# Kernel optimization log

Hardware: AMD Instinct MI355X
Metric: run time of the kernel (lower is better)

The kernel has to match this reference:

```python
import jax, jax.numpy as jnp
import numpy as np

B, S, D_IN = 1, 2048, 2048
H, KV, HD = 32, 8, 64          # num_heads, num_kv_groups, head_dim
GS = H // KV                    # group_size
D_OUT = H * HD
EPS = 1e-6


def _rmsnorm(x, w):
    # RMSNormQwen over last dim (head_dim)
    var = jnp.mean(x * x, axis=-1, keepdims=True)
    return x * jax.lax.rsqrt(var + EPS) * w


def _rope(x, cos, sin):
    # rotate-half RoPE; x: [B, heads, S, HD], cos/sin: [S, HD]
    d = x.shape[-1]
    x1, x2 = x[..., : d // 2], x[..., d // 2 :]
    rot = jnp.concatenate([-x2, x1], axis=-1)
    return x * cos + rot * sin


def setup_inputs() -> dict:
    key = jax.random.key(0)
    ks = jax.random.split(key, 8)
    x = jax.random.normal(ks[0], (B, S, D_IN), dtype=jnp.float32)
    Wq = jax.random.normal(ks[1], (D_IN, D_OUT), dtype=jnp.float32) * 0.02
    Wk = jax.random.normal(ks[2], (D_IN, KV * HD), dtype=jnp.float32) * 0.02
    Wv = jax.random.normal(ks[3], (D_IN, KV * HD), dtype=jnp.float32) * 0.02
    Wo = jax.random.normal(ks[4], (D_OUT, D_IN), dtype=jnp.float32) * 0.02
    q_norm_w = jnp.ones((HD,), dtype=jnp.float32)
    k_norm_w = jnp.ones((HD,), dtype=jnp.float32)
    # causal mask: True where masked (j > i)
    mask = jnp.triu(jnp.ones((S, S), dtype=bool), k=1)
    # RoPE tables
    inv_freq = 1.0 / (10000.0 ** (np.arange(0, HD, 2, dtype=np.float32) / HD))
    ang = np.arange(S, dtype=np.float32)[:, None] * inv_freq[None, :]  # [S, HD/2]
    cos = jnp.asarray(np.concatenate([np.cos(ang), np.cos(ang)], axis=-1))
    sin = jnp.asarray(np.concatenate([np.sin(ang), np.sin(ang)], axis=-1))
    return {"x": x, "mask": mask, "cos": cos, "sin": sin,
            "Wq": Wq, "Wk": Wk, "Wv": Wv, "Wo": Wo,
            "q_norm_w": q_norm_w, "k_norm_w": k_norm_w}


def reference(x, mask, cos, sin, Wq, Wk, Wv, Wo, q_norm_w, k_norm_w):
    b, s, _ = x.shape
    q = (x @ Wq).reshape(b, s, H, HD).transpose(0, 2, 1, 3)   # [B,H,S,HD]
    k = (x @ Wk).reshape(b, s, KV, HD).transpose(0, 2, 1, 3)  # [B,KV,S,HD]
    v = (x @ Wv).reshape(b, s, KV, HD).transpose(0, 2, 1, 3)  # [B,KV,S,HD]
    q = _rmsnorm(q, q_norm_w)
    k = _rmsnorm(k, k_norm_w)
    q = _rope(q, cos, sin)
    k = _rope(k, cos, sin)
    # grouped-KV attention without materializing repeated K/V
    qg = q.reshape(b, KV, GS, s, HD)
    scores = jnp.einsum('bkgsd,bktd->bkgst', qg, k)           # [B,KV,GS,S,S]
    scores = jnp.where(mask, -jnp.inf, scores)
    weights = jax.nn.softmax(scores / (HD ** 0.5), axis=-1)
    ctx = jnp.einsum('bkgst,bktd->bkgsd', weights, v)         # [B,KV,GS,S,HD]
    ctx = ctx.reshape(b, H, s, HD).transpose(0, 2, 1, 3).reshape(b, s, D_OUT)
    return ctx @ Wo
```

## Files before the change

### kernel.cpp

```cpp
#include <hip/hip_runtime.h>
#include <hip/hip_bf16.h>
#include <math.h>

#define S_LEN 2048
#define DIN   2048
#define NH    32
#define NKV   8
#define HD    64
#define DOUT  2048
#define QKVN  3072
#define KOFF  2048
#define VOFF  2560

typedef __attribute__((ext_vector_type(8))) short short8v;
typedef __attribute__((ext_vector_type(8))) unsigned short ushort8v;
typedef __attribute__((ext_vector_type(4))) unsigned short ushort4v;
typedef __attribute__((ext_vector_type(4))) float float4v;
typedef __attribute__((ext_vector_type(16))) float float16v;

__device__ __forceinline__ float bf2f(unsigned short u) {
    union { float f; unsigned u; } c; c.u = ((unsigned)u) << 16; return c.f;
}
__device__ __forceinline__ unsigned short f2bf(float f) {
    union { float f; unsigned u; } c; c.f = f;
    unsigned r = c.u + 0x7fffu + ((c.u >> 16) & 1u);
    return (unsigned short)(r >> 16);
}
__device__ __forceinline__ unsigned short f2h(float f) {
    union { _Float16 h; unsigned short u; } c; c.h = (_Float16)f; return c.u;
}
__device__ __forceinline__ float h2f(unsigned short u) {
    union { _Float16 h; unsigned short u; } c; c.u = u; return (float)c.h;
}
__device__ __forceinline__ unsigned cvtpk(float lo, float hi) {
    unsigned r;
    asm("v_cvt_pk_bf16_f32 %0, %1, %2" : "=v"(r) : "v"(lo), "v"(hi));
    return r;
}

__global__ __launch_bounds__(256) void prep(const float* __restrict__ Wq,
                                            const float* __restrict__ Wk,
                                            const float* __restrict__ Wv,
                                            const float* __restrict__ Wo,
                                            const float* __restrict__ x,
                                            unsigned short* __restrict__ W1,
                                            unsigned short* __restrict__ WoT,
                                            unsigned short* __restrict__ XB) {
    __shared__ float t[32][33];
    const int a = blockIdx.x;
    const int tx = threadIdx.x & 31, ty = threadIdx.x >> 5;
    if (a < 6144) {
        const int n0 = (a % 96) * 32, k0 = (a / 96) * 32;
        const float* src; int nn0, Nsrc;
        if (n0 < KOFF)      { src = Wq; nn0 = n0;        Nsrc = DOUT; }
        else if (n0 < VOFF) { src = Wk; nn0 = n0 - KOFF; Nsrc = 512; }
        else                { src = Wv; nn0 = n0 - VOFF; Nsrc = 512; }
#pragma unroll
        for (int j = ty; j < 32; j += 8)
            t[j][tx] = src[(size_t)(k0 + j) * Nsrc + nn0 + tx];
        __syncthreads();
#pragma unroll
        for (int j = ty; j < 32; j += 8)
            W1[(size_t)(n0 + j) * DIN + k0 + tx] = f2bf(t[tx][j]);
    } else if (a < 10240) {
        const int b = a - 6144;
        const int n0 = (b % 64) * 32, k0 = (b / 64) * 32;
#pragma unroll
        for (int j = ty; j < 32; j += 8)
            t[j][tx] = Wo[(size_t)(k0 + j) * DIN + n0 + tx];
        __syncthreads();
#pragma unroll
        for (int j = ty; j < 32; j += 8)
            WoT[(size_t)(n0 + j) * DOUT + k0 + tx] = f2bf(t[tx][j]);
    } else {
        const int i = (a - 10240) * 1024 + threadIdx.x * 4;
        float4 v = *(const float4*)(x + i);
        XB[i + 0] = f2bf(v.x); XB[i + 1] = f2bf(v.y);
        XB[i + 2] = f2bf(v.z); XB[i + 3] = f2bf(v.w);
    }
}

template <int FUSE>
__global__ __launch_bounds__(256) void gemm64(const unsigned short* __restrict__ A,
                                              const unsigned short* __restrict__ Bt,
                                              void* __restrict__ Cv, int M, int N, int K,
                                              const float* __restrict__ qnw,
                                              const float* __restrict__ knw,
                                              const float* __restrict__ cosb,
                                              const float* __restrict__ sinb) {
    __shared__ __attribute__((aligned(16))) unsigned short As[128 * 32];
    __shared__ __attribute__((aligned(16))) unsigned short Bs[64 * 32];
    const int tid = threadIdx.x, lane = tid & 63, w = tid >> 6;
    const int bm = blockIdx.y * 128, bn = blockIdx.x * 64;
    const int wm = w * 32;

    float4v acc[2][4];
#pragma unroll
    for (int i = 0; i < 2; i++)
#pragma unroll
        for (int j = 0; j < 4; j++) acc[i][j] = (float4v){0.f, 0.f, 0.f, 0.f};

    const int lr = lane >> 2, lc = (lane & 3) * 8;
    const unsigned short* Ag0 = A + (size_t)(bm + w * 32 + lr) * K + lc;
    const unsigned short* Ag1 = Ag0 + (size_t)16 * K;
    const unsigned short* Bg  = Bt + (size_t)(bn + w * 16 + lr) * K + lc;
    unsigned short* Al0 = As + (w * 32) * 32;
    unsigned short* Al1 = As + (w * 32 + 16) * 32;
    unsigned short* Bl  = Bs + (w * 16) * 32;

    const int frow = lane & 15, fk = (lane >> 4) * 8;

    for (int k0 = 0; k0 < K; k0 += 32) {
        __syncthreads();
        __builtin_amdgcn_global_load_lds(
            (const __attribute__((address_space(1))) void*)(Ag0 + k0),
            (__attribute__((address_space(3))) void*)Al0, 16, 0, 0);
        __builtin_amdgcn_global_load_lds(
            (const __attribute__((address_space(1))) void*)(Ag1 + k0),
            (__attribute__((address_space(3))) void*)Al1, 16, 0, 0);
        __builtin_amdgcn_global_load_lds(
            (const __attribute__((address_space(1))) void*)(Bg + k0),
            (__attribute__((address_space(3))) void*)Bl, 16, 0, 0);
        __syncthreads();

        short8v af[2], bf[4];
#pragma unroll
        for (int fm = 0; fm < 2; fm++)
            af[fm] = *(const short8v*)(As + (wm + fm * 16 + frow) * 32 + fk);
#pragma unroll
        for (int fn = 0; fn < 4; fn++)
            bf[fn] = *(const short8v*)(Bs + (fn * 16 + frow) * 32 + fk);
#pragma unroll
        for (int fm = 0; fm < 2; fm++)
#pragma unroll
            for (int fn = 0; fn < 4; fn++)
                acc[fm][fn] = __builtin_amdgcn_mfma_f32_16x16x32_bf16(
                    af[fm], bf[fn], acc[fm][fn], 0, 0, 0);
    }

    const int quad = lane >> 4, col16 = lane & 15;
    if constexpr (FUSE == 1) {
        unsigned short* C = (unsigned short*)Cv;
        const int head = bn >> 6;
        if (head < 40) {
            const float* nw = (head < 32) ? qnw : knw;
            float wv[4];
#pragma unroll
            for (int fn = 0; fn < 4; fn++) wv[fn] = nw[fn * 16 + col16];
#pragma unroll
            for (int fm = 0; fm < 2; fm++)
#pragma unroll
                for (int r = 0; r < 4; r++) {
                    float x0 = acc[fm][0][r], x1 = acc[fm][1][r];
                    float x2 = acc[fm][2][r], x3 = acc[fm][3][r];
                    float ss = x0 * x0 + x1 * x1 + x2 * x2 + x3 * x3;
                    ss += __shfl_xor(ss, 1); ss += __shfl_xor(ss, 2);
                    ss += __shfl_xor(ss, 4); ss += __shfl_xor(ss, 8);
                    const float inv = rsqrtf(ss * (1.0f / 64.0f) + 1e-6f);
                    float xn[4] = {x0 * inv * wv[0], x1 * inv * wv[1],
                                   x2 * inv * wv[2], x3 * inv * wv[3]};
                    const int row = bm + wm + fm * 16 + quad * 4 + r;
                    const float* cr = cosb + (size_t)row * HD;
                    const float* sr = sinb + (size_t)row * HD;
#pragma unroll
                    for (int fn = 0; fn < 4; fn++) {
                        const float rot = (fn < 2) ? -xn[fn + 2] : xn[fn - 2];
                        const float res = xn[fn] * cr[fn * 16 + col16] +
                                          rot * sr[fn * 16 + col16];
                        C[(size_t)row * N + bn + fn * 16 + col16] = f2bf(res);
                    }
                }
        } else {
#pragma unroll
            for (int fm = 0; fm < 2; fm++)
#pragma unroll
                for (int fn = 0; fn < 4; fn++)
#pragma unroll
                    for (int r = 0; r < 4; r++)
                        C[(size_t)(bm + wm + fm * 16 + quad * 4 + r) * N +
                          bn + fn * 16 + col16] = f2bf(acc[fm][fn][r]);
        }
    } else {
        float* C = (float*)Cv;
#pragma unroll
        for (int fm = 0; fm < 2; fm++)
#pragma unroll
            for (int fn = 0; fn < 4; fn++)
#pragma unroll
                for (int r = 0; r < 4; r++)
                    C[(size_t)(bm + wm + fm * 16 + quad * 4 + r) * N +
                      bn + fn * 16 + col16] = acc[fm][fn][r];
    }
}

#define KSTR 88

__global__ __launch_bounds__(256) void flash_part(const unsigned short* __restrict__ qb,
                                                  const unsigned short* __restrict__ kb,
                                                  const unsigned short* __restrict__ vb,
                                                  unsigned short* __restrict__ Op,
                                                  float* __restrict__ Lp) {
    __shared__ __attribute__((aligned(16))) unsigned short Ks[64 * KSTR];
    __shared__ __attribute__((aligned(16))) unsigned short Vt[64 * KSTR];

    const int tid = threadIdx.x, lane = tid & 63, w = tid >> 6;
    const int sl = lane & 31, hi = lane >> 5, hi8 = hi * 8;
    const int bid = blockIdx.x;
    const int g = bid & 7;
    const int p = (bid >> 3) & 31;
    const int s = bid >> 8;
    const int h = g * 4 + w;

    const int s0a = p * 32, s0b = (63 - p) * 32;
    const int nta = (s0a + 95) >> 6;
    const int nA  = s ? 0 : nta;
    const int bLo = s ? (17 - nta) : 0;
    const int nB  = s ? 16 : (17 - nta);
    const int nT  = nA + nB;

    const float C1 = 0.18033688011112042f;
    const float C2 = 12.262908856239697f;

    unsigned short* Oh = Op + (size_t)s * S_LEN * DOUT;
    float* Lh = Lp + (size_t)s * S_LEN * NH;

    int s0 = nA ? s0a : s0b;

    short8v qf[4];
#pragma unroll
    for (int ksq = 0; ksq < 4; ksq++)
        qf[ksq] = *(const short8v*)(qb + (size_t)(s0 + sl) * QKVN + h * HD +
                                    ksq * 16 + hi8);

    float16v O[2];
#pragma unroll
    for (int df = 0; df < 2; df++)
#pragma unroll
        for (int r = 0; r < 16; r++) O[df][r] = 0.f;
    float lsum = 0.f;

    const int kkey = tid >> 2, kch = tid & 3;
    const unsigned short* kg = kb + (size_t)kkey * QKVN + g * HD + kch * 16;
    const int vkey = tid & 63, vdb = tid >> 6;
    const unsigned short* vg = vb + (size_t)vkey * QKVN + g * HD + vdb * 16;

    auto epi = [&](int sbase) {
        float lt = lsum + __shfl_xor(lsum, 32);
        if (hi == 0) Lh[(size_t)(sbase + sl) * NH + h] = lt;
#pragma unroll
        for (int df = 0; df < 2; df++)
#pragma unroll
            for (int r = 0; r < 16; r++) {
                const int row = sbase + (r & 3) + 8 * (r >> 2) + 4 * hi;
                Oh[(size_t)row * DOUT + h * HD + df * 32 + sl] = f2h(O[df][r]);
            }
    };

    const int it0 = nA ? 0 : bLo;
    const size_t p0 = (size_t)it0 * 64 * QKVN;
    ushort8v ka0 = *(const ushort8v*)(kg + p0);
    ushort8v ka1 = *(const ushort8v*)(kg + p0 + 8);
    ushort8v va0 = *(const ushort8v*)(vg + p0);
    ushort8v va1 = *(const ushort8v*)(vg + p0 + 8);

    for (int j = 0; j < nT; j++) {
        if (j > 0) __syncthreads();
        {
            unsigned short* kd = Ks + kkey * KSTR + kch * 16;
            *(ushort8v*)kd = ka0;
            *(ushort8v*)(kd + 8) = ka1;
            unsigned short* vd = Vt + (size_t)(vdb * 16) * KSTR + vkey;
#pragma unroll
            for (int jj = 0; jj < 8; jj++) vd[jj * KSTR] = va0[jj];
#pragma unroll
            for (int jj = 0; jj < 8; jj++) vd[(8 + jj) * KSTR] = va1[jj];
        }
        __syncthreads();
        if (j + 1 < nT) {
            const int itn = (j + 1 < nA) ? (j + 1) : (bLo + (j + 1 - nA));
            const size_t off = (size_t)itn * 64 * QKVN;
            ka0 = *(const ushort8v*)(kg + off);
            ka1 = *(const ushort8v*)(kg + off + 8);
            va0 = *(const ushort8v*)(vg + off);
            va1 = *(const ushort8v*)(vg + off + 8);
        }
        if (nA && j == nA) {
            epi(s0a);
#pragma unroll
            for (int df = 0; df < 2; df++)
#pragma unroll
                for (int r = 0; r < 16; r++) O[df][r] = 0.f;
            lsum = 0.f;
            s0 = s0b;
#pragma unroll
            for (int ksq = 0; ksq < 4; ksq++)
                qf[ksq] = *(const short8v*)(qb + (size_t)(s0b + sl) * QKVN +
                                            h * HD + ksq * 16 + hi8);
        }

        const int it = (j < nA) ? j : (bLo + (j - nA));
        const int t0 = it * 64;
        const bool edge = (t0 + 63 > s0);

#pragma unroll
        for (int b = 0; b < 2; b++) {
            short8v kf[4];
#pragma unroll
            for (int ksq = 0; ksq < 4; ksq++)
                kf[ksq] = *(const short8v*)(Ks + (32 * b + sl) * KSTR +
                                            ksq * 16 + hi8);
            float16v sct;
#pragma unroll
            for (int r = 0; r < 16; r++) sct[r] = 0.f;
#pragma unroll
            for (int ksq = 0; ksq < 4; ksq++)
                sct = __builtin_amdgcn_mfma_f32_32x32x16_bf16(kf[ksq], qf[ksq],
                                                              sct, 0, 0, 0);
#pragma unroll
            for (int r = 0; r < 16; r++) {
                float arg = sct[r] * C1 - C2;
                if (edge) {
                    const int kglob = t0 + 32 * b + (r & 3) + 8 * (r >> 2) + 4 * hi;
                    arg = (kglob <= s0 + sl) ? arg : -100.f;
                }
                const float pv = exp2f(arg);
                sct[r] = pv;
                lsum += pv;
            }
            unsigned pk[8];
#pragma unroll
            for (int i = 0; i < 8; i++) pk[i] = cvtpk(sct[2 * i], sct[2 * i + 1]);
#pragma unroll
            for (int kk = 0; kk < 2; kk++) {
                const unsigned x0 = pk[4 * kk + 0], x1 = pk[4 * kk + 1];
                const unsigned y0 = pk[4 * kk + 2], y1 = pk[4 * kk + 3];
                const unsigned a0 = __shfl_xor(x0, 32), a1 = __shfl_xor(x1, 32);
                const unsigned b0 = __shfl_xor(y0, 32), b1 = __shfl_xor(y1, 32);
                union { unsigned u[4]; short8v v; } pa;
                pa.u[0] = hi ? b0 : x0;
                pa.u[1] = hi ? b1 : x1;
                pa.u[2] = hi ? y0 : a0;
                pa.u[3] = hi ? y1 : a1;
                const int ks = 2 * b + kk;
#pragma unroll
                for (int df = 0; df < 2; df++) {
                    const short8v vf = *(const short8v*)(Vt + (size_t)(df * 32 + sl) * KSTR +
                                                         ks * 16 + hi8);
                    O[df] = __builtin_amdgcn_mfma_f32_32x32x16_bf16(pa.v, vf,
                                                                    O[df], 0, 0, 0);
                }
            }
        }
    }

    epi(s0);
}

__global__ __launch_bounds__(256) void combine(unsigned short* O01,
                                               const float* __restrict__ Lp) {
    const int i4 = (blockIdx.x * 256 + threadIdx.x) * 4;
    const int srow = i4 >> 11, hh = (i4 & 2047) >> 6;
    float l = Lp[(size_t)srow * NH + hh];
    ushort4v o0 = *(const ushort4v*)(O01 + i4);
    float acc[4];
#pragma unroll
    for (int j = 0; j < 4; j++) acc[j] = h2f(o0[j]);
    if (srow >= 1024) {
        l += Lp[(size_t)S_LEN * NH + (size_t)srow * NH + hh];
        ushort4v o1 = *(const ushort4v*)(O01 + (size_t)S_LEN * DOUT + i4);
#pragma unroll
        for (int j = 0; j < 4; j++) acc[j] += h2f(o1[j]);
    }
    const float inv = 1.0f / l;
    ushort4v r;
#pragma unroll
    for (int j = 0; j < 4; j++) r[j] = f2bf(acc[j] * inv);
    *(ushort4v*)(O01 + i4) = r;
}

extern "C" void kernel_launch(void* const* d_in, const int* in_sizes, int n_in,
                              void* d_out, int out_size, void* d_ws, size_t ws_size,
                              hipStream_t stream) {
    const float* x    = (const float*)d_in[0];
    const float* cosb = (const float*)d_in[2];
    const float* sinb = (const float*)d_in[3];
    const float* Wq   = (const float*)d_in[4];
    const float* Wk   = (const float*)d_in[5];
    const float* Wv   = (const float*)d_in[6];
    const float* Wo   = (const float*)d_in[7];
    const float* qw   = (const float*)d_in[8];
    const float* kw   = (const float*)d_in[9];
    float* out = (float*)d_out;

    unsigned short* W1  = (unsigned short*)d_ws;
    unsigned short* XB  = W1 + (size_t)QKVN * DIN;
    unsigned short* WoT = XB + (size_t)S_LEN * DIN;
    unsigned short* QKV = WoT + (size_t)DIN * DOUT;
    unsigned short* Op  = (unsigned short*)d_ws;
    float*          Lp  = (float*)(Op + (size_t)2 * S_LEN * DOUT);
    unsigned short* CTX = Op;

    dim3 blk256(256);

    prep<<<dim3(14336), blk256, 0, stream>>>(Wq, Wk, Wv, Wo, x, W1, WoT, XB);

    gemm64<1><<<dim3(QKVN / 64, S_LEN / 128), blk256, 0, stream>>>(
        XB, W1, QKV, S_LEN, QKVN, DIN, qw, kw, cosb, sinb);

    flash_part<<<dim3(NKV * 32 * 2), blk256, 0, stream>>>(
        QKV, QKV + KOFF, QKV + VOFF, Op, Lp);

    combine<<<dim3(S_LEN * DOUT / 1024), blk256, 0, stream>>>(Op, Lp);

    gemm64<0><<<dim3(DIN / 64, S_LEN / 128), blk256, 0, stream>>>(
        CTX, WoT, out, S_LEN, DIN, DOUT, nullptr, nullptr, nullptr, nullptr);
}
```

Measured before the change: 264.8 us.

## Double-buffer GEMM LDS tiles with BK=64, XOR swizzle, and async prefetch

Rewrites the gemm64 main loop to stage 64-wide K tiles into two LDS buffers, prefetching the next tile via global_load_lds while MFMAs run on the current one, with manual waitcnt/barriers. The LDS layout uses an XOR swizzle of 16-byte chunks to avoid bank conflicts on fragment reads, and MFMA issue gets raised priority. This cuts barrier count per K and hides global latency, at the cost of four times the LDS per block, which may reduce occupancy.

```diff
diff --git a/kernel.cpp b/kernel.cpp
--- a/kernel.cpp
+++ b/kernel.cpp
@@ -88,8 +88,8 @@
                                               const float* __restrict__ knw,
                                               const float* __restrict__ cosb,
                                               const float* __restrict__ sinb) {
-    __shared__ __attribute__((aligned(16))) unsigned short As[128 * 32];
-    __shared__ __attribute__((aligned(16))) unsigned short Bs[64 * 32];
+    __shared__ __attribute__((aligned(16))) unsigned short As[2 * 128 * 64];
+    __shared__ __attribute__((aligned(16))) unsigned short Bs[2 * 64 * 64];
     const int tid = threadIdx.x, lane = tid & 63, w = tid >> 6;
     const int bm = blockIdx.y * 128, bn = blockIdx.x * 64;
     const int wm = w * 32;
@@ -100,45 +100,83 @@
 #pragma unroll
         for (int j = 0; j < 4; j++) acc[i][j] = (float4v){0.f, 0.f, 0.f, 0.f};
 
-    const int lr = lane >> 2, lc = (lane & 3) * 8;
-    const unsigned short* Ag0 = A + (size_t)(bm + w * 32 + lr) * K + lc;
-    const unsigned short* Ag1 = Ag0 + (size_t)16 * K;
-    const unsigned short* Bg  = Bt + (size_t)(bn + w * 16 + lr) * K + lc;
-    unsigned short* Al0 = As + (w * 32) * 32;
-    unsigned short* Al1 = As + (w * 32 + 16) * 32;
-    unsigned short* Bl  = Bs + (w * 16) * 32;
-
-    const int frow = lane & 15, fk = (lane >> 4) * 8;
-
-    for (int k0 = 0; k0 < K; k0 += 32) {
-        __syncthreads();
-        __builtin_amdgcn_global_load_lds(
-            (const __attribute__((address_space(1))) void*)(Ag0 + k0),
-            (__attribute__((address_space(3))) void*)Al0, 16, 0, 0);
-        __builtin_amdgcn_global_load_lds(
-            (const __attribute__((address_space(1))) void*)(Ag1 + k0),
-            (__attribute__((address_space(3))) void*)Al1, 16, 0, 0);
-        __builtin_amdgcn_global_load_lds(
-            (const __attribute__((address_space(1))) void*)(Bg + k0),
-            (__attribute__((address_space(3))) void*)Bl, 16, 0, 0);
-        __syncthreads();
-
-        short8v af[2], bf[4];
+    const int srow = lane >> 3;
+    const int schk = (lane & 7) ^ srow;
+    const unsigned short* Ag[4];
+    const unsigned short* Bg[2];
+#pragma unroll
+    for (int g = 0; g < 4; g++)
+        Ag[g] = A + (size_t)(bm + w * 32 + g * 8 + srow) * K + schk * 8;
+#pragma unroll
+    for (int g = 0; g < 2; g++)
+        Bg[g] = Bt + (size_t)(bn + w * 16 + g * 8 + srow) * K + schk * 8;
+
+    auto STAGE = [&](int t, int b) {
+        const size_t ko = (size_t)t * 64;
+        unsigned short* Ad = As + b * (128 * 64) + (w * 32) * 64;
+        unsigned short* Bd = Bs + b * (64 * 64) + (w * 16) * 64;
+#pragma unroll
+        for (int g = 0; g < 4; g++)
+            __builtin_amdgcn_global_load_lds(
+                (const __attribute__((address_space(1))) void*)(Ag[g] + ko),
+                (__attribute__((address_space(3))) void*)(Ad + g * 8 * 64), 16, 0, 0);
+#pragma unroll
+        for (int g = 0; g < 2; g++)
+            __builtin_amdgcn_global_load_lds(
+                (const __attribute__((address_space(1))) void*)(Bg[g] + ko),
+                (__attribute__((address_space(3))) void*)(Bd + g * 8 * 64), 16, 0, 0);
+    };
+
+    const int frow = lane & 15, quad = lane >> 4, sw = frow & 7;
+    const int NT = K >> 6;
+
+    STAGE(0, 0);
+
+    for (int t = 0; t < NT; t++) {
+        const int c = t & 1;
+        if (t + 1 < NT) {
+            STAGE(t + 1, c ^ 1);
+            asm volatile("s_waitcnt vmcnt(6)" ::: "memory");
+        } else {
+            asm volatile("s_waitcnt vmcnt(0)" ::: "memory");
+        }
+        __builtin_amdgcn_s_barrier();
+        __builtin_amdgcn_sched_barrier(0);
+
+        const unsigned short* Ab = As + c * (128 * 64);
+        const unsigned short* Bb = Bs + c * (64 * 64);
+        short8v af[2][2], bf[4][2];
 #pragma unroll
         for (int fm = 0; fm < 2; fm++)
-            af[fm] = *(const short8v*)(As + (wm + fm * 16 + frow) * 32 + fk);
+#pragma unroll
+            for (int ks = 0; ks < 2; ks++)
+                af[fm][ks] = *(const short8v*)(Ab + (wm + fm * 16 + frow) * 64 +
+                                               (((ks * 4 + quad) ^ sw) * 8));
 #pragma unroll
         for (int fn = 0; fn < 4; fn++)
-            bf[fn] = *(const short8v*)(Bs + (fn * 16 + frow) * 32 + fk);
-#pragma unroll
-        for (int fm = 0; fm < 2; fm++)
-#pragma unroll
-            for (int fn = 0; fn < 4; fn++)
-                acc[fm][fn] = __builtin_amdgcn_mfma_f32_16x16x32_bf16(
-                    af[fm], bf[fn], acc[fm][fn], 0, 0, 0);
+#pragma unroll
+            for (int ks = 0; ks < 2; ks++)
+                bf[fn][ks] = *(const short8v*)(Bb + (fn * 16 + frow) * 64 +
+                                               (((ks * 4 + quad) ^ sw) * 8));
+        __builtin_amdgcn_s_setprio(1);
+#pragma unroll
+        for (int ks = 0; ks < 2; ks++)
+#pragma unroll
+            for (int fm = 0; fm < 2; fm++)
+#pragma unroll
+                for (int fn = 0; fn < 4; fn++)
+                    acc[fm][fn] = __builtin_amdgcn_mfma_f32_16x16x32_bf16(
+                        af[fm][ks], bf[fn][ks], acc[fm][fn], 0, 0, 0);
+        __builtin_amdgcn_s_setprio(0);
+
+        if (t + 1 < NT) {
+            asm volatile("s_waitcnt lgkmcnt(0)" ::: "memory");
+            __builtin_amdgcn_sched_barrier(0);
+            __builtin_amdgcn_s_barrier();
+        }
     }
 
-    const int quad = lane >> 4, col16 = lane & 15;
+    const int quad4 = lane >> 4, col16 = lane & 15;
     if constexpr (FUSE == 1) {
         unsigned short* C = (unsigned short*)Cv;
         const int head = bn >> 6;
@@ -159,7 +197,7 @@
                     const float inv = rsqrtf(ss * (1.0f / 64.0f) + 1e-6f);
                     float xn[4] = {x0 * inv * wv[0], x1 * inv * wv[1],
                                    x2 * inv * wv[2], x3 * inv * wv[3]};
-                    const int row = bm + wm + fm * 16 + quad * 4 + r;
+                    const int row = bm + wm + fm * 16 + quad4 * 4 + r;
                     const float* cr = cosb + (size_t)row * HD;
                     const float* sr = sinb + (size_t)row * HD;
 #pragma unroll
@@ -177,7 +215,7 @@
                 for (int fn = 0; fn < 4; fn++)
 #pragma unroll
                     for (int r = 0; r < 4; r++)
-                        C[(size_t)(bm + wm + fm * 16 + quad * 4 + r) * N +
+                        C[(size_t)(bm + wm + fm * 16 + quad4 * 4 + r) * N +
                           bn + fn * 16 + col16] = f2bf(acc[fm][fn][r]);
         }
     } else {
@@ -188,7 +226,7 @@
             for (int fn = 0; fn < 4; fn++)
 #pragma unroll
                 for (int r = 0; r < 4; r++)
-                    C[(size_t)(bm + wm + fm * 16 + quad * 4 + r) * N +
+                    C[(size_t)(bm + wm + fm * 16 + quad4 * 4 + r) * N +
                       bn + fn * 16 + col16] = acc[fm][fn][r];
     }
 }
```

Measured after the change: 236.6 us. 1.12x faster.
